# Kernel optimization log

Hardware: AMD Instinct MI355X
Metric: run time of the kernel (lower is better)

Reference implementation:

```python
import jax, jax.numpy as jnp
import numpy as np

B, Q, K, QS, KS, VD, H = 4, 512, 1024, 256, 256, 256, 128
NEG = -1e9


def setup_inputs() -> dict:
    key = jax.random.key(0)
    k1, k2, k3, k4, k5, k6, k7 = jax.random.split(key, 7)
    return {
        "queries": jax.random.normal(k1, (B, Q, QS), dtype=jnp.float32),
        "keys": jax.random.normal(k2, (B, K, KS), dtype=jnp.float32),
        "values": jax.random.normal(k3, (B, K, VD), dtype=jnp.float32),
        "valid_lens": jax.random.randint(k4, (B,), 1, K + 1, dtype=jnp.int32),
        "W_q": jax.random.normal(k5, (QS, H), dtype=jnp.float32) / np.sqrt(QS),
        "W_k": jax.random.normal(k6, (KS, H), dtype=jnp.float32) / np.sqrt(KS),
        "w_v": jax.random.normal(k7, (H,), dtype=jnp.float32) / np.sqrt(H),
    }


def reference(queries, keys, values, valid_lens, W_q, W_k, w_v):
    q = jnp.einsum("bqd,dh->bqh", queries, W_q)              # (B,Q,H)
    k = jnp.einsum("bkd,dh->bkh", keys, W_k)                 # (B,K,H)
    feats = jnp.tanh(q[:, :, None, :] + k[:, None, :, :])    # (B,Q,K,H)
    scores = jnp.einsum("bqkh,h->bqk", feats, w_v)           # (B,Q,K)
    # mask: positions >= valid_len are invalid
    valid = jnp.arange(keys.shape[1])[None, None, :] < valid_lens[:, None, None]
    scores = jnp.where(valid, scores, NEG)
    attn = jax.nn.softmax(scores, axis=-1)
    return jnp.einsum("bqk,bkv->bqv", attn, values)          # (B,Q,VD)
```

## Files before the change

kernel.cpp:

```cpp
#include <hip/hip_runtime.h>

#define B_  4
#define Q_  512
#define K_  1024
#define D_  256
#define VD_ 256
#define H_  128
#define NK_ (B_*K_)

constexpr float CE  = 2.8853900817779268f;
constexpr float L2E = 1.4426950408889634f;

__device__ __forceinline__ float arcp(float x) { return __builtin_amdgcn_rcpf(x); }

__global__ __launch_bounds__(256) void proj_kernel(
    const float* __restrict__ keys, const float* __restrict__ queries,
    const float* __restrict__ Wk, const float* __restrict__ Wq,
    float* __restrict__ EkT2, float* __restrict__ Eq)
{
    __shared__ __align__(16) float Xs[8 * D_];
    __shared__ __align__(16) float Es[8][132];
    const int tid = threadIdx.x;
    const int wg  = blockIdx.x;
    const bool isK = (wg < 512);
    const float* X = isK ? (keys + (size_t)wg * 8 * D_)
                         : (queries + (size_t)(wg - 512) * 8 * D_);
    const float* W = isK ? Wk : Wq;

    {
        const float4* xg = (const float4*)X;
        ((float4*)Xs)[tid]       = xg[tid];
        ((float4*)Xs)[tid + 256] = xg[tid + 256];
    }
    __syncthreads();

    const int c    = tid & 127;
    const int half = tid >> 7;
    const float* xb = Xs + half * 4 * D_;
    float a0 = 0.f, a1 = 0.f, a2 = 0.f, a3 = 0.f;
    #pragma unroll 4
    for (int d = 0; d < D_; d += 4) {
        float w0 = W[(d+0)*H_ + c];
        float w1 = W[(d+1)*H_ + c];
        float w2 = W[(d+2)*H_ + c];
        float w3 = W[(d+3)*H_ + c];
        float4 x0 = *(const float4*)(xb + 0*D_ + d);
        float4 x1 = *(const float4*)(xb + 1*D_ + d);
        float4 x2 = *(const float4*)(xb + 2*D_ + d);
        float4 x3 = *(const float4*)(xb + 3*D_ + d);
        a0 = fmaf(x0.x,w0,a0); a0 = fmaf(x0.y,w1,a0); a0 = fmaf(x0.z,w2,a0); a0 = fmaf(x0.w,w3,a0);
        a1 = fmaf(x1.x,w0,a1); a1 = fmaf(x1.y,w1,a1); a1 = fmaf(x1.z,w2,a1); a1 = fmaf(x1.w,w3,a1);
        a2 = fmaf(x2.x,w0,a2); a2 = fmaf(x2.y,w1,a2); a2 = fmaf(x2.z,w2,a2); a2 = fmaf(x2.w,w3,a2);
        a3 = fmaf(x3.x,w0,a3); a3 = fmaf(x3.y,w1,a3); a3 = fmaf(x3.z,w2,a3); a3 = fmaf(x3.w,w3,a3);
    }
    a0 = exp2f(a0 * CE); a1 = exp2f(a1 * CE);
    a2 = exp2f(a2 * CE); a3 = exp2f(a3 * CE);

    if (isK) {
        const int r4 = half * 4;
        Es[r4+0][c] = a0; Es[r4+1][c] = a1; Es[r4+2][c] = a2; Es[r4+3][c] = a3;
        __syncthreads();
        const int h4 = tid >> 3;
        const int r  = tid & 7;
        float4 v = *(const float4*)&Es[r][h4 * 4];
        const int kg = wg * 8 + r;
        *(float4*)(EkT2 + (size_t)h4 * (NK_*4) + (size_t)kg * 4) = v;
    } else {
        const int r0 = (wg - 512) * 8 + half * 4;
        Eq[(size_t)(r0+0)*H_ + c] = a0;
        Eq[(size_t)(r0+1)*H_ + c] = a1;
        Eq[(size_t)(r0+2)*H_ + c] = a2;
        Eq[(size_t)(r0+3)*H_ + c] = a3;
    }
}

#define TERM(ACC, W_, E_, QV) ACC = fmaf(W_, arcp(fmaf(E_, QV, 1.0f)), ACC)
#define PVA(OO, P, V) { OO.x = fmaf(P, V.x, OO.x); OO.y = fmaf(P, V.y, OO.y); \
                        OO.z = fmaf(P, V.z, OO.z); OO.w = fmaf(P, V.w, OO.w); }

__global__ __launch_bounds__(1024, 8) void attn_kernel(
    const float* __restrict__ Eq, const float* __restrict__ EkT2,
    const float* __restrict__ wv, const float* __restrict__ values,
    const int* __restrict__ vlens, float* __restrict__ out)
{
    __shared__ __align__(16) float S[4][K_];
    __shared__ __align__(16) float OP[8][4][VD_/4][4];
    __shared__ __align__(16) float Eq_s[4][H_];
    __shared__ __align__(16) float msc[H_];
    __shared__ float SL[8][4];
    const int tid = threadIdx.x;
    const int wg  = blockIdx.x;
    const int y   = wg & 3;
    const int x   = wg >> 2;
    const int b   = (y + (x >> 6)) & 3;
    const int q0  = x * 4;
    const int valid = vlens[b];
    const int n   = ((valid + 255) >> 8) << 8;

    if (tid < 128) {
        msc[tid] = -2.0f * wv[tid];
        ((float4*)Eq_s)[tid] = ((const float4*)(Eq + (size_t)(b*Q_ + q0) * H_))[tid];
    }
    __syncthreads();

    const int k = tid;
    if (k < n) {
        const float4* ekp = (const float4*)EkT2 + (size_t)(b*K_ + k);
        float a0 = 0.f, a1 = 0.f, a2 = 0.f, a3 = 0.f;
        #pragma unroll 4
        for (int h4 = 0; h4 < H_/4; ++h4) {
            float4 e   = ekp[(size_t)h4 * NK_];
            float4 wv4 = *(const float4*)&msc[h4*4];
            float4 v0  = *(const float4*)&Eq_s[0][h4*4];
            float4 v1  = *(const float4*)&Eq_s[1][h4*4];
            float4 v2  = *(const float4*)&Eq_s[2][h4*4];
            float4 v3  = *(const float4*)&Eq_s[3][h4*4];
            TERM(a0,wv4.x,e.x,v0.x); TERM(a0,wv4.y,e.y,v0.y); TERM(a0,wv4.z,e.z,v0.z); TERM(a0,wv4.w,e.w,v0.w);
            TERM(a1,wv4.x,e.x,v1.x); TERM(a1,wv4.y,e.y,v1.y); TERM(a1,wv4.z,e.z,v1.z); TERM(a1,wv4.w,e.w,v1.w);
            TERM(a2,wv4.x,e.x,v2.x); TERM(a2,wv4.y,e.y,v2.y); TERM(a2,wv4.z,e.z,v2.z); TERM(a2,wv4.w,e.w,v2.w);
            TERM(a3,wv4.x,e.x,v3.x); TERM(a3,wv4.y,e.y,v3.y); TERM(a3,wv4.z,e.z,v3.z); TERM(a3,wv4.w,e.w,v3.w);
        }
        const bool ok = (k < valid);
        S[0][k] = ok ? exp2f(a0 * L2E) : 0.f;
        S[1][k] = ok ? exp2f(a1 * L2E) : 0.f;
        S[2][k] = ok ? exp2f(a2 * L2E) : 0.f;
        S[3][k] = ok ? exp2f(a3 * L2E) : 0.f;
    }
    __syncthreads();

    const int w    = tid >> 6;
    const int lane = tid & 63;
    if (w < 8) {
        const int len = n >> 3;
        const int i0  = w * len;
        float4 o0 = make_float4(0,0,0,0), o1 = o0, o2 = o0, o3 = o0;
        float l0 = 0.f, l1 = 0.f, l2 = 0.f, l3 = 0.f;
        const float4* vp = (const float4*)(values + (size_t)b * K_ * VD_);
        for (int i = i0; i < i0 + len; i += 4) {
            float4 p0 = *(const float4*)&S[0][i];
            float4 p1 = *(const float4*)&S[1][i];
            float4 p2 = *(const float4*)&S[2][i];
            float4 p3 = *(const float4*)&S[3][i];
            const float4* vr = vp + (size_t)i * (VD_/4) + lane;
            float4 va = vr[0], vb = vr[64], vc = vr[128], vd = vr[192];
            PVA(o0,p0.x,va) PVA(o0,p0.y,vb) PVA(o0,p0.z,vc) PVA(o0,p0.w,vd)
            PVA(o1,p1.x,va) PVA(o1,p1.y,vb) PVA(o1,p1.z,vc) PVA(o1,p1.w,vd)
            PVA(o2,p2.x,va) PVA(o2,p2.y,vb) PVA(o2,p2.z,vc) PVA(o2,p2.w,vd)
            PVA(o3,p3.x,va) PVA(o3,p3.y,vb) PVA(o3,p3.z,vc) PVA(o3,p3.w,vd)
            l0 += (p0.x + p0.y) + (p0.z + p0.w);
            l1 += (p1.x + p1.y) + (p1.z + p1.w);
            l2 += (p2.x + p2.y) + (p2.z + p2.w);
            l3 += (p3.x + p3.y) + (p3.z + p3.w);
        }
        *(float4*)&OP[w][0][lane][0] = o0;
        *(float4*)&OP[w][1][lane][0] = o1;
        *(float4*)&OP[w][2][lane][0] = o2;
        *(float4*)&OP[w][3][lane][0] = o3;
        if (lane == 0) { SL[w][0] = l0; SL[w][1] = l1; SL[w][2] = l2; SL[w][3] = l3; }
    }
    __syncthreads();

    if (w < 4) {
        const int row = w;
        float l = 0.f;
        #pragma unroll
        for (int s = 0; s < 8; ++s) l += SL[s][row];
        const float invl = arcp(l);
        float4 o = make_float4(0,0,0,0);
        #pragma unroll
        for (int s = 0; s < 8; ++s) {
            float4 p = *(const float4*)&OP[s][row][lane][0];
            o.x += p.x; o.y += p.y; o.z += p.z; o.w += p.w;
        }
        o.x *= invl; o.y *= invl; o.z *= invl; o.w *= invl;
        ((float4*)(out + (size_t)(b*Q_ + q0 + row) * VD_))[lane] = o;
    }
}

extern "C" void kernel_launch(void* const* d_in, const int* in_sizes, int n_in,
                              void* d_out, int out_size, void* d_ws, size_t ws_size,
                              hipStream_t stream) {
    const float* queries = (const float*)d_in[0];
    const float* keys    = (const float*)d_in[1];
    const float* values  = (const float*)d_in[2];
    const int*   vlens   = (const int*)d_in[3];
    const float* W_q     = (const float*)d_in[4];
    const float* W_k     = (const float*)d_in[5];
    const float* w_v     = (const float*)d_in[6];
    float* out = (float*)d_out;
    float* ws  = (float*)d_ws;

    float* EkT2 = ws;
    float* Eq   = ws + 524288;

    proj_kernel<<<dim3(768), dim3(256), 0, stream>>>(keys, queries, W_k, W_q, EkT2, Eq);
    attn_kernel<<<dim3((B_*Q_)/4), dim3(1024), 0, stream>>>(Eq, EkT2, w_v, values, vlens, out);
}
```

Before: 115.4 us.

## Spread PV accumulation across all sixteen waves with tree reduction

The probability-times-values phase now runs on all 16 waves of the workgroup instead of 8, each handling half as many keys. Per-wave partial outputs are merged through shared memory in a two-step tree reduction. The softmax denominators are now computed with wave shuffles while the scores are produced, rather than inside the PV loop. The aim is more memory-level parallelism on the value loads and less idle time for half the waves, at the cost of extra barriers and shared-memory traffic.

```diff
diff --git a/kernel.cpp b/kernel.cpp
--- a/kernel.cpp
+++ b/kernel.cpp
@@ -77,6 +77,7 @@
 #define TERM(ACC, W_, E_, QV) ACC = fmaf(W_, arcp(fmaf(E_, QV, 1.0f)), ACC)
 #define PVA(OO, P, V) { OO.x = fmaf(P, V.x, OO.x); OO.y = fmaf(P, V.y, OO.y); \
                         OO.z = fmaf(P, V.z, OO.z); OO.w = fmaf(P, V.w, OO.w); }
+#define ACC4(OO, P) { float4 _p = P; OO.x += _p.x; OO.y += _p.y; OO.z += _p.z; OO.w += _p.w; }
 
 __global__ __launch_bounds__(1024, 8) void attn_kernel(
     const float* __restrict__ Eq, const float* __restrict__ EkT2,
@@ -87,7 +88,7 @@
     __shared__ __align__(16) float OP[8][4][VD_/4][4];
     __shared__ __align__(16) float Eq_s[4][H_];
     __shared__ __align__(16) float msc[H_];
-    __shared__ float SL[8][4];
+    __shared__ float SL[16][4];
     const int tid = threadIdx.x;
     const int wg  = blockIdx.x;
     const int y   = wg & 3;
@@ -101,7 +102,11 @@
         msc[tid] = -2.0f * wv[tid];
         ((float4*)Eq_s)[tid] = ((const float4*)(Eq + (size_t)(b*Q_ + q0) * H_))[tid];
     }
-    __syncthreads();
+    if (tid < 64) SL[tid >> 2][tid & 3] = 0.f;
+    __syncthreads();
+
+    const int w    = tid >> 6;
+    const int lane = tid & 63;
 
     const int k = tid;
     if (k < n) {
@@ -121,54 +126,77 @@
             TERM(a3,wv4.x,e.x,v3.x); TERM(a3,wv4.y,e.y,v3.y); TERM(a3,wv4.z,e.z,v3.z); TERM(a3,wv4.w,e.w,v3.w);
         }
         const bool ok = (k < valid);
-        S[0][k] = ok ? exp2f(a0 * L2E) : 0.f;
-        S[1][k] = ok ? exp2f(a1 * L2E) : 0.f;
-        S[2][k] = ok ? exp2f(a2 * L2E) : 0.f;
-        S[3][k] = ok ? exp2f(a3 * L2E) : 0.f;
-    }
-    __syncthreads();
-
-    const int w    = tid >> 6;
-    const int lane = tid & 63;
+        float p0 = ok ? exp2f(a0 * L2E) : 0.f;
+        float p1 = ok ? exp2f(a1 * L2E) : 0.f;
+        float p2 = ok ? exp2f(a2 * L2E) : 0.f;
+        float p3 = ok ? exp2f(a3 * L2E) : 0.f;
+        S[0][k] = p0; S[1][k] = p1; S[2][k] = p2; S[3][k] = p3;
+        #pragma unroll
+        for (int off = 32; off > 0; off >>= 1) {
+            p0 += __shfl_xor(p0, off, 64); p1 += __shfl_xor(p1, off, 64);
+            p2 += __shfl_xor(p2, off, 64); p3 += __shfl_xor(p3, off, 64);
+        }
+        if (lane == 0) { SL[w][0] = p0; SL[w][1] = p1; SL[w][2] = p2; SL[w][3] = p3; }
+    }
+    __syncthreads();
+
+    const int len = n >> 4;
+    const int i0  = w * len;
+    float4 o0 = make_float4(0,0,0,0), o1 = o0, o2 = o0, o3 = o0;
+    const float4* vp = (const float4*)(values + (size_t)b * K_ * VD_);
+    for (int i = i0; i < i0 + len; i += 4) {
+        float4 p0 = *(const float4*)&S[0][i];
+        float4 p1 = *(const float4*)&S[1][i];
+        float4 p2 = *(const float4*)&S[2][i];
+        float4 p3 = *(const float4*)&S[3][i];
+        const float4* vr = vp + (size_t)i * (VD_/4) + lane;
+        float4 va = vr[0], vb = vr[64], vc = vr[128], vd = vr[192];
+        PVA(o0,p0.x,va) PVA(o0,p0.y,vb) PVA(o0,p0.z,vc) PVA(o0,p0.w,vd)
+        PVA(o1,p1.x,va) PVA(o1,p1.y,vb) PVA(o1,p1.z,vc) PVA(o1,p1.w,vd)
+        PVA(o2,p2.x,va) PVA(o2,p2.y,vb) PVA(o2,p2.z,vc) PVA(o2,p2.w,vd)
+        PVA(o3,p3.x,va) PVA(o3,p3.y,vb) PVA(o3,p3.z,vc) PVA(o3,p3.w,vd)
+    }
+
+    if (w >= 8) {
+        *(float4*)&OP[w-8][0][lane][0] = o0;
+        *(float4*)&OP[w-8][1][lane][0] = o1;
+        *(float4*)&OP[w-8][2][lane][0] = o2;
+        *(float4*)&OP[w-8][3][lane][0] = o3;
+    }
+    __syncthreads();
     if (w < 8) {
-        const int len = n >> 3;
-        const int i0  = w * len;
-        float4 o0 = make_float4(0,0,0,0), o1 = o0, o2 = o0, o3 = o0;
-        float l0 = 0.f, l1 = 0.f, l2 = 0.f, l3 = 0.f;
-        const float4* vp = (const float4*)(values + (size_t)b * K_ * VD_);
-        for (int i = i0; i < i0 + len; i += 4) {
-            float4 p0 = *(const float4*)&S[0][i];
-            float4 p1 = *(const float4*)&S[1][i];
-            float4 p2 = *(const float4*)&S[2][i];
-            float4 p3 = *(const float4*)&S[3][i];
-            const float4* vr = vp + (size_t)i * (VD_/4) + lane;
-            float4 va = vr[0], vb = vr[64], vc = vr[128], vd = vr[192];
-            PVA(o0,p0.x,va) PVA(o0,p0.y,vb) PVA(o0,p0.z,vc) PVA(o0,p0.w,vd)
-            PVA(o1,p1.x,va) PVA(o1,p1.y,vb) PVA(o1,p1.z,vc) PVA(o1,p1.w,vd)
-            PVA(o2,p2.x,va) PVA(o2,p2.y,vb) PVA(o2,p2.z,vc) PVA(o2,p2.w,vd)
-            PVA(o3,p3.x,va) PVA(o3,p3.y,vb) PVA(o3,p3.z,vc) PVA(o3,p3.w,vd)
-            l0 += (p0.x + p0.y) + (p0.z + p0.w);
-            l1 += (p1.x + p1.y) + (p1.z + p1.w);
-            l2 += (p2.x + p2.y) + (p2.z + p2.w);
-            l3 += (p3.x + p3.y) + (p3.z + p3.w);
-        }
+        ACC4(o0, (*(const float4*)&OP[w][0][lane][0]));
+        ACC4(o1, (*(const float4*)&OP[w][1][lane][0]));
+        ACC4(o2, (*(const float4*)&OP[w][2][lane][0]));
+        ACC4(o3, (*(const float4*)&OP[w][3][lane][0]));
+    }
+    if (w >= 4 && w < 8) {
         *(float4*)&OP[w][0][lane][0] = o0;
         *(float4*)&OP[w][1][lane][0] = o1;
         *(float4*)&OP[w][2][lane][0] = o2;
         *(float4*)&OP[w][3][lane][0] = o3;
-        if (lane == 0) { SL[w][0] = l0; SL[w][1] = l1; SL[w][2] = l2; SL[w][3] = l3; }
-    }
-    __syncthreads();
-
+    }
+    __syncthreads();
+    if (w < 4) {
+        ACC4(o0, (*(const float4*)&OP[w+4][0][lane][0]));
+        ACC4(o1, (*(const float4*)&OP[w+4][1][lane][0]));
+        ACC4(o2, (*(const float4*)&OP[w+4][2][lane][0]));
+        ACC4(o3, (*(const float4*)&OP[w+4][3][lane][0]));
+        *(float4*)&OP[w][0][lane][0] = o0;
+        *(float4*)&OP[w][1][lane][0] = o1;
+        *(float4*)&OP[w][2][lane][0] = o2;
+        *(float4*)&OP[w][3][lane][0] = o3;
+    }
+    __syncthreads();
     if (w < 4) {
         const int row = w;
         float l = 0.f;
         #pragma unroll
-        for (int s = 0; s < 8; ++s) l += SL[s][row];
+        for (int s = 0; s < 16; ++s) l += SL[s][row];
         const float invl = arcp(l);
         float4 o = make_float4(0,0,0,0);
         #pragma unroll
-        for (int s = 0; s < 8; ++s) {
+        for (int s = 0; s < 4; ++s) {
             float4 p = *(const float4*)&OP[s][row][lane][0];
             o.x += p.x; o.y += p.y; o.z += p.z; o.w += p.w;
         }
```

Measured after the change: 116.4 us. No clear change (+0.9%).
